# Performance work log

Hardware: AMD Instinct MI355X
Metric: run time of the kernel (lower is better)

## Reference

```python
import jax, jax.numpy as jnp
import numpy as np

N_GRAPHS = 8192
NODES_PER_GRAPH = 62
IN_CH = 4
HID = 64
NUM_CLASSES = 3
DEG = 8
N = N_GRAPHS * NODES_PER_GRAPH        # 507904 total nodes
E = N * DEG                            # 4063232 edges
BN_EPS = 1e-5


def setup_inputs() -> dict:
    key = jax.random.key(0)
    ks = jax.random.split(key, 24)

    def lin_w(k, i, o):
        return (jax.random.normal(k, (i, o), jnp.float32) / np.float32(np.sqrt(i)))

    inp = {
        "x": jax.random.normal(ks[0], (N, IN_CH), jnp.float32),
        "edge_src": jax.random.randint(ks[1], (E,), 0, N, dtype=jnp.int32),
        "edge_dst": jax.random.randint(ks[2], (E,), 0, N, dtype=jnp.int32),
        "num_graphs": N_GRAPHS,
        # conv1 MLP: Linear(4,64) -> ReLU -> Linear(64,64)
        "W1a": lin_w(ks[3], IN_CH, HID), "b1a": jnp.zeros((HID,), jnp.float32),
        "W1b": lin_w(ks[4], HID, HID),   "b1b": jnp.zeros((HID,), jnp.float32),
        "g1": jnp.ones((HID,), jnp.float32), "be1": jnp.zeros((HID,), jnp.float32),
        # conv2 MLP
        "W2a": lin_w(ks[5], HID, HID), "b2a": jnp.zeros((HID,), jnp.float32),
        "W2b": lin_w(ks[6], HID, HID), "b2b": jnp.zeros((HID,), jnp.float32),
        "g2": jnp.ones((HID,), jnp.float32), "be2": jnp.zeros((HID,), jnp.float32),
        # conv3 MLP
        "W3a": lin_w(ks[7], HID, HID), "b3a": jnp.zeros((HID,), jnp.float32),
        "W3b": lin_w(ks[8], HID, HID), "b3b": jnp.zeros((HID,), jnp.float32),
        "g3": jnp.ones((HID,), jnp.float32), "be3": jnp.zeros((HID,), jnp.float32),
        # final classifier fc2 (fc1 is unused in the original forward)
        "Wfc": lin_w(ks[9], HID, NUM_CLASSES), "bfc": jnp.zeros((NUM_CLASSES,), jnp.float32),
    }
    return inp


def _gin_conv(x, src, dst, Wa, ba, Wb, bb):
    # GINConv with eps=0: mlp(x_i + sum_{j->i} x_j)
    agg = jax.ops.segment_sum(x[src], dst, num_segments=N)
    h = x + agg
    return jnp.maximum(h @ Wa + ba, 0.0) @ Wb + bb


def _bn(h, g, b):
    # BatchNorm1d with batch statistics (training-mode math)
    m = h.mean(axis=0)
    v = h.var(axis=0)
    return (h - m) * jax.lax.rsqrt(v + BN_EPS) * g + b


def reference(x, edge_src, edge_dst, num_graphs,
              W1a, b1a, W1b, b1b, g1, be1,
              W2a, b2a, W2b, b2b, g2, be2,
              W3a, b3a, W3b, b3b, g3, be3,
              Wfc, bfc):
    h = _bn(jnp.maximum(_gin_conv(x, edge_src, edge_dst, W1a, b1a, W1b, b1b), 0.0), g1, be1)
    h = _bn(jnp.maximum(_gin_conv(h, edge_src, edge_dst, W2a, b2a, W2b, b2b), 0.0), g2, be2)
    h = _bn(jnp.maximum(_gin_conv(h, edge_src, edge_dst, W3a, b3a, W3b, b3b), 0.0), g3, be3)
    h = h.reshape(num_graphs, -1, HID).sum(axis=1)   # sum-pool nodes per graph
    # dropout is identity in eval mode
    return h @ Wfc + bfc
```

## Files before the change

kernel.cpp:

```cpp
#include <hip/hip_runtime.h>
#include <hip/hip_bf16.h>

#define NN   507904
#define NE   4063232
#define NG   8192
#define NPG  62
#define NPBLK 1984

#define NB    248
#define BRNG  2048
#define BCAP  17152
#define PBCAP 31744
#define P3BLK 992
#define CSRSZ (NB * PBCAP)

#define OFF_R     0
#define OFF_GSUM  (OFF_R + NN * 32 + 64)
#define OFF_PART  (OFF_GSUM + NG * 64)
#define OFF_AGGBF (OFF_R + NN * 64)
#define OFF_CSR   (OFF_AGGBF + NN * 32 + 32)
#define OFF_OC    (OFF_CSR + CSRSZ)
#define OFF_BCUR  (OFF_OC + 2 * NN)
#define OFF_WTB   (OFF_BCUR + 256)
#define OFF_SS    (OFF_WTB + 11264)

#define WB_W1B 0
#define WB_W2A 4096
#define WB_W2B 8192
#define WB_W3A 12288
#define WB_W3B 16384
#define WB_W1A 20480

typedef __attribute__((ext_vector_type(8))) short short8;
typedef __attribute__((ext_vector_type(4))) float f32x4;
typedef unsigned short ushort_t;

__device__ __forceinline__ ushort_t f2bf_bits(float f) {
  union { float f; unsigned u; } x; x.f = f;
  unsigned r = x.u + 0x7FFF + ((x.u >> 16) & 1);
  return (ushort_t)(r >> 16);
}
__device__ __forceinline__ float bfu(ushort_t u) {
  union { unsigned i; float f; } x; x.i = ((unsigned)u) << 16; return x.f;
}

__global__ __launch_bounds__(256) void prep_weights(
    const float* __restrict__ w1a, const float* __restrict__ w1b,
    const float* __restrict__ w2a, const float* __restrict__ w2b,
    const float* __restrict__ w3a, const float* __restrict__ w3b,
    ushort_t* __restrict__ wtb, int* __restrict__ bcur,
    unsigned* __restrict__ sent1, unsigned* __restrict__ sent2,
    float* __restrict__ gsum) {
  int b = blockIdx.x, tid = threadIdx.x;
  if (b == 0) {
    ushort_t* d = wtb + WB_W1A;
    for (int i = tid; i < 2048; i += 256) {
      int n = i >> 5, k = i & 31;
      d[i] = (k < 4) ? f2bf_bits(w1a[k * 64 + n]) : (ushort_t)0;
    }
  } else if (b == 6) {
    bcur[tid] = 0;
    if (tid < 32) { sent1[tid] = 0; sent2[tid] = 0; }
  } else if (b >= 7) {
    float* g = gsum + (size_t)(b - 7) * 1024;
#pragma unroll
    for (int k = 0; k < 4; ++k) g[k * 256 + tid] = 0.0f;
  } else {
    const float* s; ushort_t* d;
    switch (b) {
      case 1: s = w1b; d = wtb + WB_W1B; break;
      case 2: s = w2a; d = wtb + WB_W2A; break;
      case 3: s = w2b; d = wtb + WB_W2B; break;
      case 4: s = w3a; d = wtb + WB_W3A; break;
      default: s = w3b; d = wtb + WB_W3B; break;
    }
    for (int i = tid; i < 4096; i += 256) {
      int k = i >> 6, n = i & 63;
      d[n * 64 + k] = f2bf_bits(s[i]);
    }
  }
}

__global__ __launch_bounds__(256) void p3_bin(
    const int* __restrict__ src, const int* __restrict__ dst,
    int* __restrict__ bcur, uint2* __restrict__ recs) {
  __shared__ int histo[256];
  __shared__ int scan_s[256];
  __shared__ int base_s[256];
  __shared__ int cur_s[256];
  __shared__ uint2 buf[4096];
  const int tid = threadIdx.x;
  const int e0 = blockIdx.x * 4096;

  histo[tid] = 0;
  __syncthreads();

  int d_[16], s_[16];
#pragma unroll
  for (int k = 0; k < 16; ++k) {
    int e = e0 + k * 256 + tid;
    d_[k] = dst[e]; s_[k] = src[e];
    atomicAdd(&histo[d_[k] >> 11], 1);
  }
  __syncthreads();

  int v = histo[tid];
  scan_s[tid] = v; __syncthreads();
  for (int s = 1; s < 256; s <<= 1) {
    int add = (tid >= s) ? scan_s[tid - s] : 0;
    __syncthreads();
    scan_s[tid] += add;
    __syncthreads();
  }
  int excl = scan_s[tid] - v;
  if (tid < NB) base_s[tid] = atomicAdd(&bcur[tid], v);
  cur_s[tid] = excl;
  histo[tid] = excl;
  __syncthreads();

#pragma unroll
  for (int k = 0; k < 16; ++k) {
    int b = d_[k] >> 11;
    int p = atomicAdd(&cur_s[b], 1);
    uint2 r; r.x = (unsigned)d_[k]; r.y = (unsigned)s_[k];
    buf[p] = r;
  }
  __syncthreads();

  for (int i = tid; i < 4096; i += 256) {
    uint2 r = buf[i];
    int b = (int)(r.x >> 11);
    int g = base_s[b] + (i - histo[b]);
    if (g < BCAP) recs[(size_t)b * BCAP + g] = r;
  }
}

__global__ __launch_bounds__(1024) void p4_build(
    const uint2* __restrict__ recs, const int* __restrict__ bcur,
    int* __restrict__ csr, int2* __restrict__ oc) {
  __shared__ int lcnt[2048];
  __shared__ int pscan[1024];
  __shared__ int sstart[2048];
  __shared__ int scur[2048];
  const int b = blockIdx.x, tid = threadIdx.x;
  int m = bcur[b]; if (m > BCAP) m = BCAP;
  const int cbase = b * PBCAP;
  const int nbase = b << 11;
  const uint2* rp = recs + (size_t)b * BCAP;

  lcnt[tid] = 0; lcnt[1024 + tid] = 0;
  __syncthreads();
  for (int i = tid; i < m; i += 1024)
    atomicAdd(&lcnt[rp[i].x & (BRNG - 1)], 1);
  __syncthreads();

  int a0 = lcnt[2 * tid], a1 = lcnt[2 * tid + 1];
  int p0 = (a0 + 7) & ~7, p1 = (a1 + 7) & ~7;
  int ps = p0 + p1;
  pscan[tid] = ps; __syncthreads();
  for (int s = 1; s < 1024; s <<= 1) {
    int add = (tid >= s) ? pscan[tid - s] : 0;
    __syncthreads();
    pscan[tid] += add;
    __syncthreads();
  }
  int e0 = pscan[tid] - ps;
  sstart[2 * tid] = e0;          scur[2 * tid] = e0;
  sstart[2 * tid + 1] = e0 + p0; scur[2 * tid + 1] = e0 + p0;
  __syncthreads();

  {
    int2 r0; r0.x = cbase + sstart[tid];        r0.y = lcnt[tid];
    int2 r1; r1.x = cbase + sstart[1024 + tid]; r1.y = lcnt[1024 + tid];
    oc[nbase + tid] = r0;
    oc[nbase + 1024 + tid] = r1;
  }
  __syncthreads();

  for (int i = tid; i < m; i += 1024) {
    uint2 r = rp[i];
    int p = atomicAdd(&scur[r.x & (BRNG - 1)], 1);
    csr[cbase + p] = (int)r.y;
  }
  __syncthreads();

#pragma unroll
  for (int k = 0; k < 2; ++k) {
    int i = k * 1024 + tid;
    int st = sstart[i], d = lcnt[i], p = (d + 7) & ~7;
    for (int q = d; q < p; ++q) csr[cbase + st + q] = NN;
  }
}

__global__ __launch_bounds__(256) void gather1(
    const float4* __restrict__ x, const int* __restrict__ csr,
    const int2* __restrict__ oc, float4* __restrict__ tout) {
  int n = blockIdx.x * 256 + threadIdx.x;
  float4 a = x[n];
  int2 oc_ = oc[n];
  int off = oc_.x, deg = oc_.y;
  const int* cp = csr + off;
  int j = 0;
  for (; j + 4 <= deg; j += 4) {
    int s0 = cp[j], s1 = cp[j + 1], s2 = cp[j + 2], s3 = cp[j + 3];
    float4 v0 = x[s0], v1 = x[s1], v2 = x[s2], v3 = x[s3];
    a.x += v0.x + v1.x + v2.x + v3.x;
    a.y += v0.y + v1.y + v2.y + v3.y;
    a.z += v0.z + v1.z + v2.z + v3.z;
    a.w += v0.w + v1.w + v2.w + v3.w;
  }
  for (; j < deg; ++j) {
    float4 v = x[cp[j]];
    a.x += v.x; a.y += v.y; a.z += v.z; a.w += v.w;
  }
  tout[n] = a;
}

__global__ __launch_bounds__(256) void mlp_l1(
    const float4* __restrict__ tin,
    const ushort_t* __restrict__ WaTb,
    const float* __restrict__ ba,
    const ushort_t* __restrict__ WbTb,
    const float* __restrict__ bb,
    ushort_t* __restrict__ routb,
    float* __restrict__ part) {
  __shared__ __align__(16) ushort_t zt[4096];
  __shared__ float red[512];
  const int tid = threadIdx.x;
  const int wave = tid >> 6, lane = tid & 63;
  const int col = lane & 15, quad = lane >> 4;

  short8 bWa1[4], bWb[2][4];
#pragma unroll
  for (int nt = 0; nt < 4; ++nt) {
    bWa1[nt] = *(const short8*)(WaTb + (nt * 16 + col) * 32 + quad * 8);
#pragma unroll
    for (int k0 = 0; k0 < 2; ++k0)
      bWb[k0][nt] = *(const short8*)(WbTb + (nt * 16 + col) * 64 + k0 * 32 + quad * 8);
  }
  float ba_n[4], bb_n[4];
#pragma unroll
  for (int nt = 0; nt < 4; ++nt) {
    ba_n[nt] = ba[nt * 16 + col];
    bb_n[nt] = bb[nt * 16 + col];
  }

  const int wbase = wave * 1024;
  float scol[4] = {0, 0, 0, 0}, qcol[4] = {0, 0, 0, 0};

  for (int it = 0; it < 4; ++it) {
    const int tile = blockIdx.x * 256 + it * 64 + wave * 16;

    f32x4 acc1[4];
#pragma unroll
    for (int nt = 0; nt < 4; ++nt) acc1[nt] = (f32x4){0.f, 0.f, 0.f, 0.f};

    float4 t4 = tin[tile + col];
    short8 az = {0, 0, 0, 0, 0, 0, 0, 0};
    if (quad == 0) {
      az[0] = (short)f2bf_bits(t4.x);
      az[1] = (short)f2bf_bits(t4.y);
      az[2] = (short)f2bf_bits(t4.z);
      az[3] = (short)f2bf_bits(t4.w);
    }
#pragma unroll
    for (int nt = 0; nt < 4; ++nt)
      acc1[nt] = __builtin_amdgcn_mfma_f32_16x16x32_bf16(az, bWa1[nt], acc1[nt], 0, 0, 0);

#pragma unroll
    for (int nt = 0; nt < 4; ++nt) {
      int oblk = nt * 2 + (col >> 3);
#pragma unroll
      for (int r = 0; r < 4; ++r) {
        int row = quad * 4 + r;
        float z = fmaxf(acc1[nt][r] + ba_n[nt], 0.0f);
        zt[wbase + row * 64 + (((oblk ^ (row & 7)) << 3) | (col & 7))] = f2bf_bits(z);
      }
    }
    short8 az0 = *(const short8*)&zt[wbase + col * 64 + ((quad ^ (col & 7)) << 3)];
    short8 az1 = *(const short8*)&zt[wbase + col * 64 + (((4 + quad) ^ (col & 7)) << 3)];

    f32x4 acc2[4];
#pragma unroll
    for (int nt = 0; nt < 4; ++nt) acc2[nt] = (f32x4){0.f, 0.f, 0.f, 0.f};
#pragma unroll
    for (int nt = 0; nt < 4; ++nt) {
      acc2[nt] = __builtin_amdgcn_mfma_f32_16x16x32_bf16(az0, bWb[0][nt], acc2[nt], 0, 0, 0);
      acc2[nt] = __builtin_amdgcn_mfma_f32_16x16x32_bf16(az1, bWb[1][nt], acc2[nt], 0, 0, 0);
    }
#pragma unroll
    for (int nt = 0; nt < 4; ++nt) {
      int oblk = nt * 2 + (col >> 3);
#pragma unroll
      for (int r = 0; r < 4; ++r) {
        int rw = quad * 4 + r;
        float v = fmaxf(acc2[nt][r] + bb_n[nt], 0.0f);
        zt[wbase + rw * 64 + (((oblk ^ (rw & 7)) << 3) | (col & 7))] = f2bf_bits(v);
        scol[nt] += v; qcol[nt] += v * v;
      }
    }
    {
      const int R = lane >> 2, sp = lane & 3;
      short8 w0 = *(const short8*)&zt[wbase + R * 64 + (((sp * 2) ^ (R & 7)) << 3)];
      short8 w1 = *(const short8*)&zt[wbase + R * 64 + (((sp * 2 + 1) ^ (R & 7)) << 3)];
      ushort_t* dst = routb + (size_t)(tile + R) * 64 + sp * 16;
      *(short8*)dst = w0;
      *(short8*)(dst + 8) = w1;
    }
  }

#pragma unroll
  for (int nt = 0; nt < 4; ++nt) {
    float s = scol[nt], q = qcol[nt];
    s += __shfl_xor(s, 16); s += __shfl_xor(s, 32);
    q += __shfl_xor(q, 16); q += __shfl_xor(q, 32);
    if (quad == 0) {
      red[wave * 128 + nt * 16 + col] = s;
      red[wave * 128 + 64 + nt * 16 + col] = q;
    }
  }
  __syncthreads();
  if (tid < 128)
    part[blockIdx.x * 128 + tid] =
        red[tid] + red[128 + tid] + red[256 + tid] + red[384 + tid];
}

template <bool GS>
__global__ __launch_bounds__(256) void mlp_fused(
    const ushort_t* __restrict__ h,
    const int* __restrict__ csr, const int2* __restrict__ oc,
    const float* __restrict__ ss,
    const ushort_t* __restrict__ WaTb,
    const float* __restrict__ ba,
    const ushort_t* __restrict__ WbTb,
    const float* __restrict__ bb,
    ushort_t* __restrict__ routb, float* __restrict__ gsum_g,
    float* __restrict__ part) {
  __shared__ __align__(16) ushort_t zt[4096];
  __shared__ float red[512];
  __shared__ float ssl[128];
  __shared__ float gsum[GS ? 384 : 1];
  const int tid = threadIdx.x;
  const int wave = tid >> 6, lane = tid & 63;
  const int col = lane & 15, quad = lane >> 4;
  if (tid < 128) ssl[tid] = ss[tid];
  const int g0 = (blockIdx.x * 256) / 62;
  if (GS) {
    for (int i = tid; i < 384; i += 256) gsum[i] = 0.0f;
  }

  short8 bWa[2][4], bWb[2][4];
#pragma unroll
  for (int nt = 0; nt < 4; ++nt) {
#pragma unroll
    for (int k0 = 0; k0 < 2; ++k0) {
      bWa[k0][nt] = *(const short8*)(WaTb + (nt * 16 + col) * 64 + k0 * 32 + quad * 8);
      bWb[k0][nt] = *(const short8*)(WbTb + (nt * 16 + col) * 64 + k0 * 32 + quad * 8);
    }
  }
  float ba_n[4], bb_n[4];
#pragma unroll
  for (int nt = 0; nt < 4; ++nt) {
    ba_n[nt] = ba[nt * 16 + col];
    bb_n[nt] = bb[nt * 16 + col];
  }
  __syncthreads();

  const float* scA = ssl + quad * 8;
  const float* scB = ssl + 32 + quad * 8;
  const float* sfA = ssl + 64 + quad * 8;
  const float* sfB = ssl + 96 + quad * 8;

  const int wbase = wave * 1024;
  float scol[4] = {0, 0, 0, 0}, qcol[4] = {0, 0, 0, 0};

  for (int it = 0; it < 4; ++it) {
    const int tile = blockIdx.x * 256 + it * 64 + wave * 16;
    const int row = tile + col;
    const int2 o = oc[row];

    const ushort_t* hp = h + (size_t)(unsigned)row * 64u + quad * 8;
    short8 sl0 = *(const short8*)hp;
    short8 sl1 = *(const short8*)(hp + 32);
    float accA[8], accB[8];
#pragma unroll
    for (int e = 0; e < 8; ++e) {
      accA[e] = bfu((ushort_t)sl0[e]);
      accB[e] = bfu((ushort_t)sl1[e]);
    }

    const int chunks = (o.y + 7) >> 3;
    for (int c = 0; c < chunks; ++c) {
      const int* cp = csr + o.x + (c << 3);
      int4 i0 = *(const int4*)cp;
      int4 i1 = *(const int4*)(cp + 4);
      int idx[8] = {i0.x, i0.y, i0.z, i0.w, i1.x, i1.y, i1.z, i1.w};
#pragma unroll
      for (int j = 0; j < 8; ++j) {
        const ushort_t* p = h + (size_t)(unsigned)idx[j] * 64u + quad * 8;
        short8 l0 = *(const short8*)p;
        short8 l1 = *(const short8*)(p + 32);
#pragma unroll
        for (int e = 0; e < 8; ++e) {
          accA[e] += bfu((ushort_t)l0[e]);
          accB[e] += bfu((ushort_t)l1[e]);
        }
      }
    }

    const float m1 = (float)(o.y + 1);
    short8 a0, a1;
#pragma unroll
    for (int e = 0; e < 8; ++e) {
      a0[e] = (short)f2bf_bits(fmaf(scA[e], accA[e], m1 * sfA[e]));
      a1[e] = (short)f2bf_bits(fmaf(scB[e], accB[e], m1 * sfB[e]));
    }

    f32x4 acc1[4];
#pragma unroll
    for (int nt = 0; nt < 4; ++nt) acc1[nt] = (f32x4){0.f, 0.f, 0.f, 0.f};
#pragma unroll
    for (int nt = 0; nt < 4; ++nt) {
      acc1[nt] = __builtin_amdgcn_mfma_f32_16x16x32_bf16(a0, bWa[0][nt], acc1[nt], 0, 0, 0);
      acc1[nt] = __builtin_amdgcn_mfma_f32_16x16x32_bf16(a1, bWa[1][nt], acc1[nt], 0, 0, 0);
    }

#pragma unroll
    for (int nt = 0; nt < 4; ++nt) {
      int oblk = nt * 2 + (col >> 3);
#pragma unroll
      for (int r = 0; r < 4; ++r) {
        int rw = quad * 4 + r;
        float z = fmaxf(acc1[nt][r] + ba_n[nt], 0.0f);
        zt[wbase + rw * 64 + (((oblk ^ (rw & 7)) << 3) | (col & 7))] = f2bf_bits(z);
      }
    }
    short8 az0 = *(const short8*)&zt[wbase + col * 64 + ((quad ^ (col & 7)) << 3)];
    short8 az1 = *(const short8*)&zt[wbase + col * 64 + (((4 + quad) ^ (col & 7)) << 3)];

    f32x4 acc2[4];
#pragma unroll
    for (int nt = 0; nt < 4; ++nt) acc2[nt] = (f32x4){0.f, 0.f, 0.f, 0.f};
#pragma unroll
    for (int nt = 0; nt < 4; ++nt) {
      acc2[nt] = __builtin_amdgcn_mfma_f32_16x16x32_bf16(az0, bWb[0][nt], acc2[nt], 0, 0, 0);
      acc2[nt] = __builtin_amdgcn_mfma_f32_16x16x32_bf16(az1, bWb[1][nt], acc2[nt], 0, 0, 0);
    }

    if (GS) {
      const int gLo = tile / 62;
      const int rEnd = (gLo + 1) * 62;
      float vLo[4], vHi[4];
#pragma unroll
      for (int nt = 0; nt < 4; ++nt) { vLo[nt] = 0.f; vHi[nt] = 0.f; }
#pragma unroll
      for (int nt = 0; nt < 4; ++nt) {
#pragma unroll
        for (int r = 0; r < 4; ++r) {
          int rw = tile + quad * 4 + r;
          float v = fmaxf(acc2[nt][r] + bb_n[nt], 0.0f);
          scol[nt] += v; qcol[nt] += v * v;
          if (rw < rEnd) vLo[nt] += v; else vHi[nt] += v;
        }
      }
#pragma unroll
      for (int nt = 0; nt < 4; ++nt) {
        vLo[nt] += __shfl_xor(vLo[nt], 16); vLo[nt] += __shfl_xor(vLo[nt], 32);
        vHi[nt] += __shfl_xor(vHi[nt], 16); vHi[nt] += __shfl_xor(vHi[nt], 32);
      }
      if (quad == 0) {
        const int gl = gLo - g0;
#pragma unroll
        for (int nt = 0; nt < 4; ++nt) {
          atomicAdd(&gsum[gl * 64 + nt * 16 + col], vLo[nt]);
          atomicAdd(&gsum[(gl + 1) * 64 + nt * 16 + col], vHi[nt]);
        }
      }
    } else {
#pragma unroll
      for (int nt = 0; nt < 4; ++nt) {
        int oblk = nt * 2 + (col >> 3);
#pragma unroll
        for (int r = 0; r < 4; ++r) {
          int rw = quad * 4 + r;
          float v = fmaxf(acc2[nt][r] + bb_n[nt], 0.0f);
          zt[wbase + rw * 64 + (((oblk ^ (rw & 7)) << 3) | (col & 7))] = f2bf_bits(v);
          scol[nt] += v; qcol[nt] += v * v;
        }
      }
      const int R = lane >> 2, sp = lane & 3;
      short8 w0 = *(const short8*)&zt[wbase + R * 64 + (((sp * 2) ^ (R & 7)) << 3)];
      short8 w1 = *(const short8*)&zt[wbase + R * 64 + (((sp * 2 + 1) ^ (R & 7)) << 3)];
      ushort_t* dst = routb + (size_t)(tile + R) * 64 + sp * 16;
      *(short8*)dst = w0;
      *(short8*)(dst + 8) = w1;
    }
  }

#pragma unroll
  for (int nt = 0; nt < 4; ++nt) {
    float s = scol[nt], q = qcol[nt];
    s += __shfl_xor(s, 16); s += __shfl_xor(s, 32);
    q += __shfl_xor(q, 16); q += __shfl_xor(q, 32);
    if (quad == 0) {
      red[wave * 128 + nt * 16 + col] = s;
      red[wave * 128 + 64 + nt * 16 + col] = q;
    }
  }
  __syncthreads();
  if (tid < 128)
    part[blockIdx.x * 128 + tid] =
        red[tid] + red[128 + tid] + red[256 + tid] + red[384 + tid];

  if (GS) {
    for (int i = tid; i < 384; i += 256) {
      int g = g0 + (i >> 6);
      float v = gsum[i];
      if (g < NG && v != 0.0f) atomicAdd(&gsum_g[(size_t)g * 64 + (i & 63)], v);
    }
  }
}

__global__ __launch_bounds__(256) void reduce_finalize(
    const float* __restrict__ part, const float* __restrict__ gma,
    const float* __restrict__ bta, float* __restrict__ ss) {
  __shared__ double sh[512];
  const int c = blockIdx.x, tid = threadIdx.x;
  double a = 0.0, b = 0.0;
  for (int blk = tid; blk < NPBLK; blk += 256) {
    a += (double)part[blk * 128 + c];
    b += (double)part[blk * 128 + 64 + c];
  }
  sh[tid] = a; sh[256 + tid] = b;
  __syncthreads();
  for (int s = 128; s; s >>= 1) {
    if (tid < s) { sh[tid] += sh[tid + s]; sh[256 + tid] += sh[256 + tid + s]; }
    __syncthreads();
  }
  if (tid == 0) {
    double mean = sh[0] / (double)NN;
    double var = sh[256] / (double)NN - mean * mean;
    double sc = (double)gma[c] / sqrt(var + 1e-5);
    ss[c] = (float)sc;
    ss[64 + c] = (float)((double)bta[c] - mean * sc);
  }
}

__global__ __launch_bounds__(256) void fc_out(
    const float* __restrict__ gsum_g, const float* __restrict__ ss,
    const float* __restrict__ wfc, const float* __restrict__ bfc,
    float* __restrict__ out) {
  const int lane = threadIdx.x & 63;
  const int g = blockIdx.x * 4 + (threadIdx.x >> 6);
  const int c = lane;
  float s = gsum_g[(size_t)g * 64 + c];
  float pooled = fmaf(ss[c], s, (float)NPG * ss[64 + c]);
#pragma unroll
  for (int j = 0; j < 3; ++j) {
    float v = pooled * wfc[c * 3 + j];
    for (int m = 32; m; m >>= 1) v += __shfl_xor(v, m);
    if (c == 0) out[g * 3 + j] = v + bfc[j];
  }
}

extern "C" void kernel_launch(void* const* d_in, const int* in_sizes, int n_in,
                              void* d_out, int out_size, void* d_ws, size_t ws_size,
                              hipStream_t stream) {
  const float* x    = (const float*)d_in[0];
  const int*   srcE = (const int*)d_in[1];
  const int*   dstE = (const int*)d_in[2];
  const float* W1a = (const float*)d_in[4],  *b1a = (const float*)d_in[5];
  const float* W1b = (const float*)d_in[6],  *b1b = (const float*)d_in[7];
  const float* g1  = (const float*)d_in[8],  *be1 = (const float*)d_in[9];
  const float* W2a = (const float*)d_in[10], *b2a = (const float*)d_in[11];
  const float* W2b = (const float*)d_in[12], *b2b = (const float*)d_in[13];
  const float* g2  = (const float*)d_in[14], *be2 = (const float*)d_in[15];
  const float* W3a = (const float*)d_in[16], *b3a = (const float*)d_in[17];
  const float* W3b = (const float*)d_in[18], *b3b = (const float*)d_in[19];
  const float* g3  = (const float*)d_in[20], *be3 = (const float*)d_in[21];
  const float* Wfc = (const float*)d_in[22], *bfc = (const float*)d_in[23];

  float* ws = (float*)d_ws;
  ushort_t* Rb     = (ushort_t*)(ws + OFF_R);
  float*    GSUM   = ws + OFF_GSUM;
  float*    PART   = ws + OFF_PART;
  ushort_t* Ab     = (ushort_t*)(ws + OFF_AGGBF);
  void*     T1     = (void*)(ws + OFF_AGGBF);
  uint2*    RECS   = (uint2*)(ws + OFF_AGGBF);
  int*      CSR    = (int*)(ws + OFF_CSR);
  int2*     OC     = (int2*)(ws + OFF_OC);
  int*      BCUR   = (int*)(ws + OFF_BCUR);
  ushort_t* WTB    = (ushort_t*)(ws + OFF_WTB);
  float*    SS     = ws + OFF_SS;

  prep_weights<<<519, 256, 0, stream>>>(W1a, W1b, W2a, W2b, W3a, W3b, WTB, BCUR,
                                        (unsigned*)(Rb + (size_t)NN * 64),
                                        (unsigned*)(Ab + (size_t)NN * 64),
                                        GSUM);

  p3_bin<<<P3BLK, 256, 0, stream>>>(srcE, dstE, BCUR, RECS);
  p4_build<<<NB, 1024, 0, stream>>>(RECS, BCUR, CSR, OC);

  gather1<<<NN / 256, 256, 0, stream>>>((const float4*)x, CSR, OC, (float4*)T1);
  mlp_l1<<<NPBLK, 256, 0, stream>>>((const float4*)T1, WTB + WB_W1A, b1a,
                                    WTB + WB_W1B, b1b, Rb, PART);
  reduce_finalize<<<64, 256, 0, stream>>>(PART, g1, be1, SS + 0);

  mlp_fused<false><<<NPBLK, 256, 0, stream>>>(Rb, CSR, OC, SS + 0,
                                              WTB + WB_W2A, b2a,
                                              WTB + WB_W2B, b2b,
                                              Ab, nullptr, PART);
  reduce_finalize<<<64, 256, 0, stream>>>(PART, g2, be2, SS + 128);

  mlp_fused<true><<<NPBLK, 256, 0, stream>>>(Ab, CSR, OC, SS + 128,
                                             WTB + WB_W3A, b3a,
                                             WTB + WB_W3B, b3b,
                                             nullptr, GSUM, PART);
  reduce_finalize<<<64, 256, 0, stream>>>(PART, g3, be3, SS + 256);

  fc_out<<<NG / 4, 256, 0, stream>>>(GSUM, SS + 256, Wfc, bfc, (float*)d_out);
}
```

Measured before the change: 570.2 us.

## Fuse layer-1 neighbor gather into MLP kernel and double rows per block

Removes the separate gather1 kernel and folds the 4-channel neighbor aggregation into the layer-1 MLP kernel. Each quad of lanes reads two edges per 8-edge CSR chunk, and the partial sums are combined with cross-lane shuffles. This drops the intermediate T1 write and read and one launch. It also halves the block count for all MLP kernels (512 rows per block, 992 blocks), enlarging the graph-sum shared buffer, which lowers parallelism but amortizes weight loading.

```diff
diff --git a/kernel.cpp b/kernel.cpp
--- a/kernel.cpp
+++ b/kernel.cpp
@@ -5,7 +5,7 @@
 #define NE   4063232
 #define NG   8192
 #define NPG  62
-#define NPBLK 1984
+#define NBLKF 992
 
 #define NB    248
 #define BRNG  2048
@@ -192,32 +192,9 @@
   }
 }
 
-__global__ __launch_bounds__(256) void gather1(
+__global__ __launch_bounds__(256) void mlp_l1f(
     const float4* __restrict__ x, const int* __restrict__ csr,
-    const int2* __restrict__ oc, float4* __restrict__ tout) {
-  int n = blockIdx.x * 256 + threadIdx.x;
-  float4 a = x[n];
-  int2 oc_ = oc[n];
-  int off = oc_.x, deg = oc_.y;
-  const int* cp = csr + off;
-  int j = 0;
-  for (; j + 4 <= deg; j += 4) {
-    int s0 = cp[j], s1 = cp[j + 1], s2 = cp[j + 2], s3 = cp[j + 3];
-    float4 v0 = x[s0], v1 = x[s1], v2 = x[s2], v3 = x[s3];
-    a.x += v0.x + v1.x + v2.x + v3.x;
-    a.y += v0.y + v1.y + v2.y + v3.y;
-    a.z += v0.z + v1.z + v2.z + v3.z;
-    a.w += v0.w + v1.w + v2.w + v3.w;
-  }
-  for (; j < deg; ++j) {
-    float4 v = x[cp[j]];
-    a.x += v.x; a.y += v.y; a.z += v.z; a.w += v.w;
-  }
-  tout[n] = a;
-}
-
-__global__ __launch_bounds__(256) void mlp_l1(
-    const float4* __restrict__ tin,
+    const int2* __restrict__ oc,
     const ushort_t* __restrict__ WaTb,
     const float* __restrict__ ba,
     const ushort_t* __restrict__ WbTb,
@@ -248,20 +225,43 @@
   const int wbase = wave * 1024;
   float scol[4] = {0, 0, 0, 0}, qcol[4] = {0, 0, 0, 0};
 
-  for (int it = 0; it < 4; ++it) {
-    const int tile = blockIdx.x * 256 + it * 64 + wave * 16;
+  for (int it = 0; it < 8; ++it) {
+    const int tile = blockIdx.x * 512 + it * 64 + wave * 16;
+    const int row = tile + col;
+    const int2 o = oc[row];
+
+    float ax = 0.f, ay = 0.f, az_ = 0.f, aw = 0.f;
+    if (quad == 0) {
+      float4 s = x[row];
+      ax = s.x; ay = s.y; az_ = s.z; aw = s.w;
+    }
+    const int chunks = (o.y + 7) >> 3;
+    for (int c = 0; c < chunks; ++c) {
+      int2 ij = *(const int2*)(csr + o.x + (c << 3) + (quad << 1));
+      if (ij.x < NN) {
+        float4 v = x[ij.x];
+        ax += v.x; ay += v.y; az_ += v.z; aw += v.w;
+      }
+      if (ij.y < NN) {
+        float4 v = x[ij.y];
+        ax += v.x; ay += v.y; az_ += v.z; aw += v.w;
+      }
+    }
+    ax += __shfl_xor(ax, 16); ax += __shfl_xor(ax, 32);
+    ay += __shfl_xor(ay, 16); ay += __shfl_xor(ay, 32);
+    az_ += __shfl_xor(az_, 16); az_ += __shfl_xor(az_, 32);
+    aw += __shfl_xor(aw, 16); aw += __shfl_xor(aw, 32);
 
     f32x4 acc1[4];
 #pragma unroll
     for (int nt = 0; nt < 4; ++nt) acc1[nt] = (f32x4){0.f, 0.f, 0.f, 0.f};
 
-    float4 t4 = tin[tile + col];
     short8 az = {0, 0, 0, 0, 0, 0, 0, 0};
     if (quad == 0) {
-      az[0] = (short)f2bf_bits(t4.x);
-      az[1] = (short)f2bf_bits(t4.y);
-      az[2] = (short)f2bf_bits(t4.z);
-      az[3] = (short)f2bf_bits(t4.w);
+      az[0] = (short)f2bf_bits(ax);
+      az[1] = (short)f2bf_bits(ay);
+      az[2] = (short)f2bf_bits(az_);
+      az[3] = (short)f2bf_bits(aw);
     }
 #pragma unroll
     for (int nt = 0; nt < 4; ++nt)
@@ -272,9 +272,9 @@
       int oblk = nt * 2 + (col >> 3);
 #pragma unroll
       for (int r = 0; r < 4; ++r) {
-        int row = quad * 4 + r;
+        int rw = quad * 4 + r;
         float z = fmaxf(acc1[nt][r] + ba_n[nt], 0.0f);
-        zt[wbase + row * 64 + (((oblk ^ (row & 7)) << 3) | (col & 7))] = f2bf_bits(z);
+        zt[wbase + rw * 64 + (((oblk ^ (rw & 7)) << 3) | (col & 7))] = f2bf_bits(z);
       }
     }
     short8 az0 = *(const short8*)&zt[wbase + col * 64 + ((quad ^ (col & 7)) << 3)];
@@ -339,14 +339,14 @@
   __shared__ __align__(16) ushort_t zt[4096];
   __shared__ float red[512];
   __shared__ float ssl[128];
-  __shared__ float gsum[GS ? 384 : 1];
+  __shared__ float gsum[GS ? 640 : 1];
   const int tid = threadIdx.x;
   const int wave = tid >> 6, lane = tid & 63;
   const int col = lane & 15, quad = lane >> 4;
   if (tid < 128) ssl[tid] = ss[tid];
-  const int g0 = (blockIdx.x * 256) / 62;
+  const int g0 = (blockIdx.x * 512) / 62;
   if (GS) {
-    for (int i = tid; i < 384; i += 256) gsum[i] = 0.0f;
+    for (int i = tid; i < 640; i += 256) gsum[i] = 0.0f;
   }
 
   short8 bWa[2][4], bWb[2][4];
@@ -374,8 +374,8 @@
   const int wbase = wave * 1024;
   float scol[4] = {0, 0, 0, 0}, qcol[4] = {0, 0, 0, 0};
 
-  for (int it = 0; it < 4; ++it) {
-    const int tile = blockIdx.x * 256 + it * 64 + wave * 16;
+  for (int it = 0; it < 8; ++it) {
+    const int tile = blockIdx.x * 512 + it * 64 + wave * 16;
     const int row = tile + col;
     const int2 o = oc[row];
 
@@ -513,7 +513,7 @@
         red[tid] + red[128 + tid] + red[256 + tid] + red[384 + tid];
 
   if (GS) {
-    for (int i = tid; i < 384; i += 256) {
+    for (int i = tid; i < 640; i += 256) {
       int g = g0 + (i >> 6);
       float v = gsum[i];
       if (g < NG && v != 0.0f) atomicAdd(&gsum_g[(size_t)g * 64 + (i & 63)], v);
@@ -527,7 +527,7 @@
   __shared__ double sh[512];
   const int c = blockIdx.x, tid = threadIdx.x;
   double a = 0.0, b = 0.0;
-  for (int blk = tid; blk < NPBLK; blk += 256) {
+  for (int blk = tid; blk < NBLKF; blk += 256) {
     a += (double)part[blk * 128 + c];
     b += (double)part[blk * 128 + 64 + c];
   }
@@ -585,7 +585,6 @@
   float*    GSUM   = ws + OFF_GSUM;
   float*    PART   = ws + OFF_PART;
   ushort_t* Ab     = (ushort_t*)(ws + OFF_AGGBF);
-  void*     T1     = (void*)(ws + OFF_AGGBF);
   uint2*    RECS   = (uint2*)(ws + OFF_AGGBF);
   int*      CSR    = (int*)(ws + OFF_CSR);
   int2*     OC     = (int2*)(ws + OFF_OC);
@@ -601,18 +600,18 @@
   p3_bin<<<P3BLK, 256, 0, stream>>>(srcE, dstE, BCUR, RECS);
   p4_build<<<NB, 1024, 0, stream>>>(RECS, BCUR, CSR, OC);
 
-  gather1<<<NN / 256, 256, 0, stream>>>((const float4*)x, CSR, OC, (float4*)T1);
-  mlp_l1<<<NPBLK, 256, 0, stream>>>((const float4*)T1, WTB + WB_W1A, b1a,
-                                    WTB + WB_W1B, b1b, Rb, PART);
+  mlp_l1f<<<NBLKF, 256, 0, stream>>>((const float4*)x, CSR, OC,
+                                     WTB + WB_W1A, b1a, WTB + WB_W1B, b1b,
+                                     Rb, PART);
   reduce_finalize<<<64, 256, 0, stream>>>(PART, g1, be1, SS + 0);
 
-  mlp_fused<false><<<NPBLK, 256, 0, stream>>>(Rb, CSR, OC, SS + 0,
+  mlp_fused<false><<<NBLKF, 256, 0, stream>>>(Rb, CSR, OC, SS + 0,
                                               WTB + WB_W2A, b2a,
                                               WTB + WB_W2B, b2b,
                                               Ab, nullptr, PART);
   reduce_finalize<<<64, 256, 0, stream>>>(PART, g2, be2, SS + 128);
 
-  mlp_fused<true><<<NPBLK, 256, 0, stream>>>(Ab, CSR, OC, SS + 128,
+  mlp_fused<true><<<NBLKF, 256, 0, stream>>>(Ab, CSR, OC, SS + 128,
                                              WTB + WB_W3A, b3a,
                                              WTB + WB_W3B, b3b,
                                              nullptr, GSUM, PART);
```

Measured after the change: 539.7 us. -5.3%, faster.
